# Performance work log

Measured on AMD Instinct MI355X. Metric: run time of the kernel, lower is better.

## Reference

```python
import jax, jax.numpy as jnp
import numpy as np

TOKEN_NUM = 81   # init default token_num
KNN_K = 2        # hardcoded in apply_clustering
LAYER_INDEX = 3


def setup_inputs() -> dict:
    key = jax.random.key(0)
    k1, k2, k3 = jax.random.split(key, 3)
    B, F, N, C = 8, 1024, 17, 512
    x = jax.random.normal(k1, (B, F, N, C), dtype=jnp.float32)
    # nn.Parameter init normal_(std=0.02)
    pos_embed_token = 0.02 * jax.random.normal(k2, (1, TOKEN_NUM, C), dtype=jnp.float32)
    # deterministic stand-in for torch.rand tie-breaker noise on density
    density_noise = jax.random.uniform(k3, (B, F), dtype=jnp.float32)
    return {"x": x, "pos_embed_token": pos_embed_token,
            "density_noise": density_noise, "current_layer": LAYER_INDEX}


def _dpc_knn_index(x_knn, density_noise, cluster_num, k):
    # x_knn: (B, F, C) pooled features; returns sorted cluster-center indices (B, cluster_num)
    B, F, C = x_knn.shape
    sq = jnp.sum(x_knn * x_knn, axis=-1)                       # (B, F)
    d2 = sq[:, :, None] + sq[:, None, :] - 2.0 * jnp.einsum('bic,bjc->bij', x_knn, x_knn)
    dist = jnp.sqrt(jnp.maximum(d2, 0.0)) / jnp.sqrt(jnp.asarray(C, x_knn.dtype))  # cdist / C**0.5
    # k smallest distances (self included, dist 0)
    neg_nearest, _ = jax.lax.top_k(-dist, k)                   # (B, F, k)
    dist_nearest = -neg_nearest
    density = jnp.exp(-jnp.mean(dist_nearest ** 2, axis=-1))   # (B, F)
    density = density + density_noise * 1e-6                   # tie-breaker
    # mask[b,i,j] = density[b,j] > density[b,i]
    mask = (density[:, None, :] > density[:, :, None]).astype(x_knn.dtype)
    dist_max = jnp.max(dist.reshape(B, -1), axis=-1)[:, None, None]
    min_dist = jnp.min(dist * mask + dist_max * (1.0 - mask), axis=-1)  # (B, F)
    score = min_dist * density
    _, index_down = jax.lax.top_k(score, cluster_num)          # (B, cluster_num)
    return jnp.sort(index_down, axis=-1)


def reference(x, pos_embed_token, density_noise, current_layer):
    # forward path only hits clustering when current_layer == layer_index
    if current_layer != LAYER_INDEX:
        return x
    B, F, N, C = x.shape
    # AdaptiveAvgPool1d(1) over joint axis after 'b f n c -> b (f c) n' == mean over n
    x_knn = jnp.mean(x, axis=2)                                # (B, F, C)
    index = _dpc_knn_index(x_knn, density_noise, TOKEN_NUM, KNN_K)
    index = jax.lax.stop_gradient(index)                       # clustering is under no_grad
    # gather selected frames: x[batch, index] -> (B, token_num, N, C)
    compressed = jnp.take_along_axis(x, index[:, :, None, None], axis=1)
    # '+ pos_embed_token' applied per (b n) f c  ==  broadcast over joints
    compressed = compressed + pos_embed_token[:, :, None, :]
    return compressed
```

## Files before the change

kernel.cpp:

```cpp
#include <hip/hip_runtime.h>
#include <math.h>
#include <float.h>

#define BB 8
#define FF 1024
#define NJ 17
#define CH 512
#define TOK 81
#define RCP_SQRT_C 0.04419417382415922f
#define LP 133

typedef short bf16x8 __attribute__((ext_vector_type(8)));
typedef float f32x16 __attribute__((ext_vector_type(16)));

static __device__ inline unsigned short f2bf(float f) {
    __bf16 h = (__bf16)f;
    return __builtin_bit_cast(unsigned short, h);
}
static __device__ inline float bf2f(unsigned short u) {
    return (float)__builtin_bit_cast(__bf16, u);
}


__global__ __launch_bounds__(256) void pool_kernel(const float* __restrict__ x,
                                                   uint4* __restrict__ fhi,
                                                   uint4* __restrict__ flo,
                                                   float* __restrict__ sq,
                                                   unsigned* __restrict__ ctrl) {
    const int t = threadIdx.x;
    if (blockIdx.x == 0 && t < 24) ctrl[t] = 0u;
    const int wid = t >> 6, lane = t & 63;
    const int row0 = blockIdx.x * 4;
    const int row = row0 + wid;
    const int b = row >> 10, f0 = row0 & 1023;
    const float* px = x + (size_t)row * NJ * CH + lane * 8;
    float a[8] = {};
    #pragma unroll
    for (int n = 0; n < NJ; ++n) {
        const float4 v0 = *(const float4*)(px + (size_t)n * CH);
        const float4 v1 = *(const float4*)(px + (size_t)n * CH + 4);
        a[0] += v0.x; a[1] += v0.y; a[2] += v0.z; a[3] += v0.w;
        a[4] += v1.x; a[5] += v1.y; a[6] += v1.z; a[7] += v1.w;
    }
    float ssq = 0.f;
    unsigned short hi[8], lo[8];
    #pragma unroll
    for (int j = 0; j < 8; ++j) {
        const float m = a[j] / 17.0f;
        ssq += m * m;
        hi[j] = f2bf(m);
        lo[j] = f2bf(m - bf2f(hi[j]));
    }
    #pragma unroll
    for (int off = 32; off > 0; off >>= 1) ssq += __shfl_down(ssq, off);
    if (lane == 0) sq[row] = ssq;

    uint4 uh, ul;
    uh.x = (unsigned)hi[0] | ((unsigned)hi[1] << 16);
    uh.y = (unsigned)hi[2] | ((unsigned)hi[3] << 16);
    uh.z = (unsigned)hi[4] | ((unsigned)hi[5] << 16);
    uh.w = (unsigned)hi[6] | ((unsigned)hi[7] << 16);
    ul.x = (unsigned)lo[0] | ((unsigned)lo[1] << 16);
    ul.y = (unsigned)lo[2] | ((unsigned)lo[3] << 16);
    ul.z = (unsigned)lo[4] | ((unsigned)lo[5] << 16);
    ul.w = (unsigned)lo[6] | ((unsigned)lo[7] << 16);
    __shared__ uint4 sh_hi[256], sh_lo[256];
    sh_hi[lane * 4 + wid] = uh;
    sh_lo[lane * 4 + wid] = ul;
    __syncthreads();
    const int k8 = t >> 2, fpr = t & 3;
    const int s = k8 >> 1, h = k8 & 1;
    const size_t o = (((size_t)b * 32 + s) * 2 + h) * 1024 + f0 + fpr;
    fhi[o] = sh_hi[t];
    flo[o] = sh_lo[t];
}

__global__ __launch_bounds__(256) void dist_kernel(const uint4* __restrict__ fhi,
                                                   const uint4* __restrict__ flo,
                                                   const float* __restrict__ sq,
                                                   float* __restrict__ dist) {
    const int b = blockIdx.x & 7;
    int tri = blockIdx.x >> 3, rt = 0;
    while (tri >= 8 - rt) { tri -= 8 - rt; ++rt; }
    const int ct = rt + tri;
    const bool diag = (rt == ct);
    const int tid = threadIdx.x;
    const int w = tid >> 6, lane = tid & 63;
    const int R = rt * 128 + (w & 1) * 64;
    const int C = ct * 128 + (w >> 1) * 64;
    const int h = lane >> 5, fr = lane & 31;

    size_t a0 = ((size_t)b * 64 + h) * 1024 + R + fr;
    size_t b0 = ((size_t)b * 64 + h) * 1024 + C + fr;

    f32x16 acc00, acc01, acc10, acc11;
    #pragma unroll
    for (int i = 0; i < 16; ++i) { acc00[i] = 0.f; acc01[i] = 0.f; acc10[i] = 0.f; acc11[i] = 0.f; }

    bf16x8 A0h = *(const bf16x8*)(fhi + a0), A1h = *(const bf16x8*)(fhi + a0 + 32);
    bf16x8 A0l = *(const bf16x8*)(flo + a0), A1l = *(const bf16x8*)(flo + a0 + 32);
    bf16x8 B0h = *(const bf16x8*)(fhi + b0), B1h = *(const bf16x8*)(fhi + b0 + 32);
    bf16x8 B0l = *(const bf16x8*)(flo + b0), B1l = *(const bf16x8*)(flo + b0 + 32);

    #pragma unroll 4
    for (int s = 0; s < 32; ++s) {
        const bf16x8 cA0h = A0h, cA1h = A1h, cA0l = A0l, cA1l = A1l;
        const bf16x8 cB0h = B0h, cB1h = B1h, cB0l = B0l, cB1l = B1l;
        if (s < 31) {
            a0 += 2048; b0 += 2048;
            A0h = *(const bf16x8*)(fhi + a0); A1h = *(const bf16x8*)(fhi + a0 + 32);
            A0l = *(const bf16x8*)(flo + a0); A1l = *(const bf16x8*)(flo + a0 + 32);
            B0h = *(const bf16x8*)(fhi + b0); B1h = *(const bf16x8*)(fhi + b0 + 32);
            B0l = *(const bf16x8*)(flo + b0); B1l = *(const bf16x8*)(flo + b0 + 32);
        }
        acc00 = __builtin_amdgcn_mfma_f32_32x32x16_bf16(cA0h, cB0h, acc00, 0, 0, 0);
        acc01 = __builtin_amdgcn_mfma_f32_32x32x16_bf16(cA0h, cB1h, acc01, 0, 0, 0);
        acc10 = __builtin_amdgcn_mfma_f32_32x32x16_bf16(cA1h, cB0h, acc10, 0, 0, 0);
        acc11 = __builtin_amdgcn_mfma_f32_32x32x16_bf16(cA1h, cB1h, acc11, 0, 0, 0);
        acc00 = __builtin_amdgcn_mfma_f32_32x32x16_bf16(cA0h, cB0l, acc00, 0, 0, 0);
        acc01 = __builtin_amdgcn_mfma_f32_32x32x16_bf16(cA0h, cB1l, acc01, 0, 0, 0);
        acc10 = __builtin_amdgcn_mfma_f32_32x32x16_bf16(cA1h, cB0l, acc10, 0, 0, 0);
        acc11 = __builtin_amdgcn_mfma_f32_32x32x16_bf16(cA1h, cB1l, acc11, 0, 0, 0);
        acc00 = __builtin_amdgcn_mfma_f32_32x32x16_bf16(cA0l, cB0h, acc00, 0, 0, 0);
        acc01 = __builtin_amdgcn_mfma_f32_32x32x16_bf16(cA0l, cB1h, acc01, 0, 0, 0);
        acc10 = __builtin_amdgcn_mfma_f32_32x32x16_bf16(cA1l, cB0h, acc10, 0, 0, 0);
        acc11 = __builtin_amdgcn_mfma_f32_32x32x16_bf16(cA1l, cB1h, acc11, 0, 0, 0);
    }

    __shared__ float lds[64 * LP];
    const int bF = b * FF;
    const int R0 = rt * 128, C0 = ct * 128;
    const float sqc0 = sq[bF + C + fr], sqc1 = sq[bF + C + fr + 32];
    const int lcb = (w >> 1) * 64 + fr;

    #pragma unroll
    for (int p = 0; p < 2; ++p) {
        if ((w & 1) == p) {
            #pragma unroll
            for (int reg = 0; reg < 16; ++reg) {
                const int rp = 4 * h + (reg & 3) + 8 * (reg >> 2);
                const float sqr0 = sq[bF + R + rp];
                const float sqr1 = sq[bF + R + rp + 32];
                lds[rp * LP + lcb] =
                    sqrtf(fmaxf(sqr0 + sqc0 - 2.0f * acc00[reg], 0.f)) * RCP_SQRT_C;
                lds[rp * LP + lcb + 32] =
                    sqrtf(fmaxf(sqr0 + sqc1 - 2.0f * acc01[reg], 0.f)) * RCP_SQRT_C;
                lds[(rp + 32) * LP + lcb] =
                    sqrtf(fmaxf(sqr1 + sqc0 - 2.0f * acc10[reg], 0.f)) * RCP_SQRT_C;
                lds[(rp + 32) * LP + lcb + 32] =
                    sqrtf(fmaxf(sqr1 + sqc1 - 2.0f * acc11[reg], 0.f)) * RCP_SQRT_C;
            }
        }
        __syncthreads();
        if (!diag) {
            for (int q = tid; q < 64 * 128; q += 256) {
                const int lr = q >> 7, c = q & 127;
                dist[((size_t)bF + R0 + p * 64 + lr) * FF + C0 + c] = lds[lr * LP + c];
            }
            for (int q = tid; q < 64 * 128; q += 256) {
                const int lr = q & 63, c = q >> 6;
                dist[((size_t)bF + C0 + c) * FF + R0 + p * 64 + lr] = lds[lr * LP + c];
            }
        } else if (p == 0) {
            for (int q = tid; q < 64 * 128; q += 256) {
                const int i = q >> 7, j = q & 127;
                const float v = (i == j) ? 0.f : (i < j ? lds[i * LP + j] : lds[j * LP + i]);
                dist[((size_t)bF + R0 + i) * FF + C0 + j] = v;
            }
            for (int q = tid; q < 64 * 64; q += 256) {
                const int i = 64 + (q >> 6), j = q & 63;
                dist[((size_t)bF + R0 + i) * FF + C0 + j] = lds[j * LP + i];
            }
        } else {
            for (int q = tid; q < 64 * 64; q += 256) {
                const int i = 64 + (q >> 6), j = 64 + (q & 63);
                const float v = (i == j) ? 0.f
                               : (i < j ? lds[(i - 64) * LP + j] : lds[(j - 64) * LP + i]);
                dist[((size_t)bF + R0 + i) * FF + C0 + j] = v;
            }
        }
        __syncthreads();
    }
}

__global__ __launch_bounds__(256) void stats_kernel(const float* __restrict__ dist,
                                                    const float* __restrict__ noise,
                                                    float* __restrict__ density,
                                                    unsigned* __restrict__ ctrl,
                                                    float* __restrict__ score,
                                                    int* __restrict__ selsort,
                                                    const float* __restrict__ x,
                                                    const float* __restrict__ pos,
                                                    float* __restrict__ out) {
    const int t = threadIdx.x, wid = t >> 6, lane = t & 63;
    const int g = blockIdx.x;
    const int b = g >> 5;
    unsigned* dmx = ctrl;
    unsigned* syncA = ctrl + 8;
    unsigned* syncD = ctrl + 9;
    unsigned* bcnt  = ctrl + 10;

    __shared__ float sdens[4][8];
    float wmax = -FLT_MAX;
    #pragma unroll
    for (int k = 0; k < 8; ++k) {
        const int r = g * 32 + wid * 8 + k;
        const int dcol = r & 1023;
        const float* dr = dist + (size_t)r * FF + lane * 4;
        float mn = FLT_MAX, mx = -FLT_MAX;
        #pragma unroll
        for (int j = 0; j < 4; ++j) {
            float4 d = *(const float4*)(dr + j * 256);
            mx = fmaxf(mx, fmaxf(fmaxf(d.x, d.y), fmaxf(d.z, d.w)));
            const int c0 = lane * 4 + j * 256;
            d.x = (c0 + 0 == dcol) ? FLT_MAX : d.x;
            d.y = (c0 + 1 == dcol) ? FLT_MAX : d.y;
            d.z = (c0 + 2 == dcol) ? FLT_MAX : d.z;
            d.w = (c0 + 3 == dcol) ? FLT_MAX : d.w;
            mn = fminf(mn, fminf(fminf(d.x, d.y), fminf(d.z, d.w)));
        }
        #pragma unroll
        for (int off = 32; off > 0; off >>= 1) {
            mn = fminf(mn, __shfl_down(mn, off));
            mx = fmaxf(mx, __shfl_down(mx, off));
        }
        if (lane == 0) {
            const float dv = expf(-0.5f * mn * mn) + noise[r] * 1e-6f;
            density[r] = dv;
            sdens[wid][k] = dv;
            wmax = fmaxf(wmax, mx);
        }
    }
    __shared__ float swm[4];
    if (lane == 0) swm[wid] = wmax;
    __syncthreads();
    if (t == 0) {
        atomicMax(&dmx[b], __float_as_uint(fmaxf(fmaxf(swm[0], swm[1]), fmaxf(swm[2], swm[3]))));
        __threadfence();
        atomicAdd(syncA, 1u);
        while (__hip_atomic_load(syncA, __ATOMIC_ACQUIRE, __HIP_MEMORY_SCOPE_AGENT) < 256u)
            __builtin_amdgcn_s_sleep(8);
    }
    __syncthreads();
    __threadfence();

    const float dmaxb = __uint_as_float(
        __hip_atomic_load(&dmx[b], __ATOMIC_RELAXED, __HIP_MEMORY_SCOPE_AGENT));
    float e[16];
    {
        const volatile float* db = density + (size_t)b * FF;
        #pragma unroll
        for (int j = 0; j < 16; ++j) e[j] = db[lane + j * 64];
    }
    #pragma unroll
    for (int k = 0; k < 8; ++k) {
        const int r = g * 32 + wid * 8 + k;
        const float dme = sdens[wid][k];
        const float* dr = dist + (size_t)r * FF;
        float mn = FLT_MAX;
        #pragma unroll
        for (int j = 0; j < 16; ++j) {
            const float d = dr[lane + j * 64];
            mn = fminf(mn, (e[j] > dme) ? d : FLT_MAX);
        }
        #pragma unroll
        for (int off = 32; off > 0; off >>= 1) mn = fminf(mn, __shfl_down(mn, off));
        if (lane == 0) score[r] = ((mn == FLT_MAX) ? dmaxb : mn) * dme;
    }
    __syncthreads();

    __shared__ int slast;
    if (t == 0) {
        __threadfence();
        slast = (atomicAdd(&bcnt[b], 1u) == 31u) ? 1 : 0;
    }
    __syncthreads();
    if (slast) {
        __threadfence();
        const volatile float* sb = score + (size_t)b * FF;
        unsigned v[4];
        #pragma unroll
        for (int j = 0; j < 4; ++j) v[j] = __float_as_uint(sb[t + 256 * j]);

        __shared__ unsigned hist[256];
        __shared__ unsigned wtot[4];
        __shared__ unsigned sh_byte, sh_kk;
        unsigned prefix = 0, kk = TOK;
        #pragma unroll
        for (int pass = 0; pass < 4; ++pass) {
            const int sh = 24 - 8 * pass;
            const unsigned pmask = (pass == 0) ? 0u : (0xFFFFFFFFu << (sh + 8));
            hist[t] = 0;
            __syncthreads();
            #pragma unroll
            for (int j = 0; j < 4; ++j)
                if ((v[j] & pmask) == prefix) atomicAdd(&hist[(v[j] >> sh) & 255], 1u);
            __syncthreads();
            const unsigned cnt = hist[t];
            unsigned s = cnt;
            #pragma unroll
            for (int off = 1; off < 64; off <<= 1) {
                const unsigned o = __shfl_down(s, off);
                if (lane + off < 64) s += o;
            }
            if (lane == 0) wtot[wid] = s;
            __syncthreads();
            unsigned hi2 = 0;
            for (int w2 = wid + 1; w2 < 4; ++w2) hi2 += wtot[w2];
            const unsigned S_incl = s + hi2;
            const unsigned S_excl = S_incl - cnt;
            if (S_excl < kk && kk <= S_incl) { sh_byte = (unsigned)t; sh_kk = kk - S_excl; }
            __syncthreads();
            prefix |= (sh_byte << sh);
            kk = sh_kk;
        }
        const unsigned T = prefix;

        __shared__ unsigned cgt[16], ceq[16];
        unsigned long long bgt[4], beq[4];
        #pragma unroll
        for (int j = 0; j < 4; ++j) {
            bgt[j] = __ballot(v[j] > T);
            beq[j] = __ballot(v[j] == T);
            if (lane == 0) {
                cgt[j * 4 + wid] = (unsigned)__popcll(bgt[j]);
                ceq[j * 4 + wid] = (unsigned)__popcll(beq[j]);
            }
        }
        __syncthreads();
        const unsigned long long below = (1ULL << lane) - 1ULL;
        #pragma unroll
        for (int j = 0; j < 4; ++j) {
            const bool gt = v[j] > T, eq = v[j] == T;
            if (!gt && !eq) continue;
            const int c = j * 4 + wid;
            unsigned bq_gt = 0, bq_eq = 0;
            for (int cc = 0; cc < c; ++cc) { bq_gt += cgt[cc]; bq_eq += ceq[cc]; }
            const unsigned wgt = (unsigned)__popcll(bgt[j] & below);
            const unsigned weq = (unsigned)__popcll(beq[j] & below);
            unsigned pos_;
            if (gt) {
                const unsigned eq_before = bq_eq + weq;
                pos_ = bq_gt + wgt + ((eq_before < kk) ? eq_before : kk);
            } else {
                const unsigned eord = bq_eq + weq;
                if (eord >= kk) continue;
                pos_ = bq_gt + wgt + eord;
            }
            selsort[b * TOK + pos_] = (int)(t + 256 * j);
        }
        __threadfence();
    }
    __syncthreads();
    if (t == 0) atomicAdd(syncD, 1u);

    if (t == 0) {
        while (__hip_atomic_load(syncD, __ATOMIC_ACQUIRE, __HIP_MEMORY_SCOPE_AGENT) < 256u)
            __builtin_amdgcn_s_sleep(8);
    }
    __syncthreads();
    __threadfence();

    __shared__ int ssel[BB * TOK];
    for (int q = t; q < BB * TOK; q += 256) ssel[q] = *((volatile const int*)selsort + q);
    __syncthreads();
    const size_t total = (size_t)BB * TOK * NJ * (CH / 4);
    for (size_t i = (size_t)g * 256 + t; i < total; i += 256 * 256) {
        const int c4 = (int)(i & (CH / 4 - 1));
        size_t r = i >> 7;
        const int n = (int)(r % NJ); r /= NJ;
        const int tok = (int)(r % TOK);
        const int bb = (int)(r / TOK);
        const int f = ssel[bb * TOK + tok];
        float4 v = *(const float4*)(x + (((size_t)(bb * FF + f)) * NJ + n) * CH + c4 * 4);
        const float4 p = *(const float4*)(pos + (size_t)tok * CH + c4 * 4);
        v.x += p.x; v.y += p.y; v.z += p.z; v.w += p.w;
        *(float4*)(out + i * 4) = v;
    }
}

extern "C" void kernel_launch(void* const* d_in, const int* in_sizes, int n_in,
                              void* d_out, int out_size, void* d_ws, size_t ws_size,
                              hipStream_t stream) {
    const float* x     = (const float*)d_in[0];
    const float* pos   = (const float*)d_in[1];
    const float* noise = (const float*)d_in[2];
    float* out = (float*)d_out;

    uint4* fhi    = (uint4*)d_ws;
    uint4* flo    = fhi + (size_t)BB * 32 * 2 * 1024;
    float* dist   = (float*)(flo + (size_t)BB * 32 * 2 * 1024);
    float* sq      = dist + (size_t)BB * FF * FF;
    float* density = sq + BB * FF;
    unsigned* ctrl = (unsigned*)(density + BB * FF);
    float* score   = (float*)(ctrl + 24);
    int*   selsort = (int*)(score + BB * FF);

    pool_kernel<<<(BB * FF) / 4, 256, 0, stream>>>(x, fhi, flo, sq, ctrl);
    dist_kernel<<<288, 256, 0, stream>>>(fhi, flo, sq, dist);
    stats_kernel<<<256, 256, 0, stream>>>(dist, noise, density, ctrl, score, selsort,
                                          x, pos, out);
}
```

Before: 563.6 us.

## Fuse nearest-neighbour min and global max into distance GEMM epilogue, split gather kernel

The distance kernel now computes each row's nearest non-self distance (via wave shuffles and atomicMin on float bits) and the per-batch maximum distance (atomicMax) directly from the MFMA accumulators. This removes the first pass over the full distance matrix and the grid-wide spin barrier from the stats kernel. The old persistent stats kernel is replaced by a per-row score kernel with a last-block top-k selection, followed by a separate fully parallel gather kernel that does not need a second grid barrier. The cost is many global atomics and an extra kernel launch.

```diff
diff --git a/kernel.cpp b/kernel.cpp
--- a/kernel.cpp
+++ b/kernel.cpp
@@ -20,17 +20,22 @@
 static __device__ inline float bf2f(unsigned short u) {
     return (float)__builtin_bit_cast(__bf16, u);
 }
+static __device__ __forceinline__ float densf(float rm, float nz) {
+    return expf(-0.5f * (rm * rm)) + nz * 1e-6f;
+}
 
 
 __global__ __launch_bounds__(256) void pool_kernel(const float* __restrict__ x,
                                                    uint4* __restrict__ fhi,
                                                    uint4* __restrict__ flo,
                                                    float* __restrict__ sq,
-                                                   unsigned* __restrict__ ctrl) {
+                                                   unsigned* __restrict__ ctrl,
+                                                   unsigned* __restrict__ rmin) {
     const int t = threadIdx.x;
-    if (blockIdx.x == 0 && t < 24) ctrl[t] = 0u;
+    const int row0 = blockIdx.x * 4;
+    if (t < 4) rmin[row0 + t] = 0x7F7FFFFFu;
+    if (blockIdx.x == 0 && t < 16) ctrl[t] = 0u;
     const int wid = t >> 6, lane = t & 63;
-    const int row0 = blockIdx.x * 4;
     const int row = row0 + wid;
     const int b = row >> 10, f0 = row0 & 1023;
     const float* px = x + (size_t)row * NJ * CH + lane * 8;
@@ -78,7 +83,9 @@
 __global__ __launch_bounds__(256) void dist_kernel(const uint4* __restrict__ fhi,
                                                    const uint4* __restrict__ flo,
                                                    const float* __restrict__ sq,
-                                                   float* __restrict__ dist) {
+                                                   float* __restrict__ dist,
+                                                   unsigned* __restrict__ ctrl,
+                                                   unsigned* __restrict__ rmin) {
     const int b = blockIdx.x & 7;
     int tri = blockIdx.x >> 3, rt = 0;
     while (tri >= 8 - rt) { tri -= 8 - rt; ++rt; }
@@ -127,10 +134,64 @@
         acc11 = __builtin_amdgcn_mfma_f32_32x32x16_bf16(cA1l, cB1h, acc11, 0, 0, 0);
     }
 
+    const int bF = b * FF;
+    const float sqc0 = sq[bF + C + fr], sqc1 = sq[bF + C + fr + 32];
+    #pragma unroll
+    for (int reg = 0; reg < 16; ++reg) {
+        const int rp = 4 * h + (reg & 3) + 8 * (reg >> 2);
+        const float sqr0 = sq[bF + R + rp];
+        const float sqr1 = sq[bF + R + rp + 32];
+        acc00[reg] = sqrtf(fmaxf(sqr0 + sqc0 - 2.0f * acc00[reg], 0.f)) * RCP_SQRT_C;
+        acc01[reg] = sqrtf(fmaxf(sqr0 + sqc1 - 2.0f * acc01[reg], 0.f)) * RCP_SQRT_C;
+        acc10[reg] = sqrtf(fmaxf(sqr1 + sqc0 - 2.0f * acc10[reg], 0.f)) * RCP_SQRT_C;
+        acc11[reg] = sqrtf(fmaxf(sqr1 + sqc1 - 2.0f * acc11[reg], 0.f)) * RCP_SQRT_C;
+    }
+
+    float mx = 0.f;
+    #pragma unroll
+    for (int reg = 0; reg < 16; ++reg) {
+        const int rp = 4 * h + (reg & 3) + 8 * (reg >> 2);
+        float w00 = acc00[reg], w01 = acc01[reg], w10 = acc10[reg], w11 = acc11[reg];
+        float x00 = w00, x01 = w01, x10 = w10, x11 = w11;
+        if (diag) {
+            if (C + fr == R + rp)           { w00 = FLT_MAX; x00 = 0.f; }
+            if (C + 32 + fr == R + rp)      { w01 = FLT_MAX; x01 = 0.f; }
+            if (C + fr == R + 32 + rp)      { w10 = FLT_MAX; x10 = 0.f; }
+            if (C + 32 + fr == R + 32 + rp) { w11 = FLT_MAX; x11 = 0.f; }
+        }
+        mx = fmaxf(mx, fmaxf(fmaxf(x00, x01), fmaxf(x10, x11)));
+        float r0 = fminf(w00, w01);
+        float r1 = fminf(w10, w11);
+        #pragma unroll
+        for (int off = 1; off < 32; off <<= 1) {
+            r0 = fminf(r0, __shfl_xor(r0, off));
+            r1 = fminf(r1, __shfl_xor(r1, off));
+        }
+        if (fr == 0) {
+            atomicMin(&rmin[bF + R + rp], __float_as_uint(r0));
+            atomicMin(&rmin[bF + R + 32 + rp], __float_as_uint(r1));
+        }
+    }
+    if (!diag) {
+        float c0 = FLT_MAX, c1 = FLT_MAX;
+        #pragma unroll
+        for (int reg = 0; reg < 16; ++reg) {
+            c0 = fminf(c0, fminf(acc00[reg], acc10[reg]));
+            c1 = fminf(c1, fminf(acc01[reg], acc11[reg]));
+        }
+        c0 = fminf(c0, __shfl_xor(c0, 32));
+        c1 = fminf(c1, __shfl_xor(c1, 32));
+        if (h == 0) {
+            atomicMin(&rmin[bF + C + fr], __float_as_uint(c0));
+            atomicMin(&rmin[bF + C + 32 + fr], __float_as_uint(c1));
+        }
+    }
+    #pragma unroll
+    for (int off = 1; off < 64; off <<= 1) mx = fmaxf(mx, __shfl_xor(mx, off));
+    if (lane == 0) atomicMax(&ctrl[b], __float_as_uint(mx));
+
     __shared__ float lds[64 * LP];
-    const int bF = b * FF;
     const int R0 = rt * 128, C0 = ct * 128;
-    const float sqc0 = sq[bF + C + fr], sqc1 = sq[bF + C + fr + 32];
     const int lcb = (w >> 1) * 64 + fr;
 
     #pragma unroll
@@ -139,16 +200,10 @@
             #pragma unroll
             for (int reg = 0; reg < 16; ++reg) {
                 const int rp = 4 * h + (reg & 3) + 8 * (reg >> 2);
-                const float sqr0 = sq[bF + R + rp];
-                const float sqr1 = sq[bF + R + rp + 32];
-                lds[rp * LP + lcb] =
-                    sqrtf(fmaxf(sqr0 + sqc0 - 2.0f * acc00[reg], 0.f)) * RCP_SQRT_C;
-                lds[rp * LP + lcb + 32] =
-                    sqrtf(fmaxf(sqr0 + sqc1 - 2.0f * acc01[reg], 0.f)) * RCP_SQRT_C;
-                lds[(rp + 32) * LP + lcb] =
-                    sqrtf(fmaxf(sqr1 + sqc0 - 2.0f * acc10[reg], 0.f)) * RCP_SQRT_C;
-                lds[(rp + 32) * LP + lcb + 32] =
-                    sqrtf(fmaxf(sqr1 + sqc1 - 2.0f * acc11[reg], 0.f)) * RCP_SQRT_C;
+                lds[rp * LP + lcb]            = acc00[reg];
+                lds[rp * LP + lcb + 32]       = acc01[reg];
+                lds[(rp + 32) * LP + lcb]     = acc10[reg];
+                lds[(rp + 32) * LP + lcb + 32] = acc11[reg];
             }
         }
         __syncthreads();
@@ -183,200 +238,174 @@
     }
 }
 
-__global__ __launch_bounds__(256) void stats_kernel(const float* __restrict__ dist,
-                                                    const float* __restrict__ noise,
-                                                    float* __restrict__ density,
-                                                    unsigned* __restrict__ ctrl,
-                                                    float* __restrict__ score,
-                                                    int* __restrict__ selsort,
-                                                    const float* __restrict__ x,
-                                                    const float* __restrict__ pos,
-                                                    float* __restrict__ out) {
+__global__ __launch_bounds__(256) void scoretop_kernel(const float* __restrict__ dist,
+                                                       const unsigned* __restrict__ rmin,
+                                                       const float* __restrict__ noise,
+                                                       unsigned* __restrict__ ctrl,
+                                                       float* __restrict__ score,
+                                                       int* __restrict__ selsort) {
     const int t = threadIdx.x, wid = t >> 6, lane = t & 63;
-    const int g = blockIdx.x;
-    const int b = g >> 5;
-    unsigned* dmx = ctrl;
-    unsigned* syncA = ctrl + 8;
-    unsigned* syncD = ctrl + 9;
-    unsigned* bcnt  = ctrl + 10;
-
-    __shared__ float sdens[4][8];
-    float wmax = -FLT_MAX;
-    #pragma unroll
-    for (int k = 0; k < 8; ++k) {
-        const int r = g * 32 + wid * 8 + k;
-        const int dcol = r & 1023;
-        const float* dr = dist + (size_t)r * FF + lane * 4;
-        float mn = FLT_MAX, mx = -FLT_MAX;
+    const int r = blockIdx.x * 4 + wid;
+    const int b = r >> 10, bF = b * FF;
+
+    float4 e0, e1, e2, e3;
+    #define MKE(EJ, J) { \
+        const uint4 rm = *(const uint4*)(rmin + bF + lane * 4 + (J) * 256); \
+        const float4 nz = *(const float4*)(noise + bF + lane * 4 + (J) * 256); \
+        EJ.x = densf(__uint_as_float(rm.x), nz.x); \
+        EJ.y = densf(__uint_as_float(rm.y), nz.y); \
+        EJ.z = densf(__uint_as_float(rm.z), nz.z); \
+        EJ.w = densf(__uint_as_float(rm.w), nz.w); }
+    MKE(e0, 0) MKE(e1, 1) MKE(e2, 2) MKE(e3, 3)
+    #undef MKE
+
+    const int dcol = r & 1023;
+    const int osel = ((dcol >> 8) << 2) | (dcol & 3);
+    const int olane = (dcol & 255) >> 2;
+    float own;
+    switch (osel) {
+        case 0:  own = e0.x; break; case 1:  own = e0.y; break;
+        case 2:  own = e0.z; break; case 3:  own = e0.w; break;
+        case 4:  own = e1.x; break; case 5:  own = e1.y; break;
+        case 6:  own = e1.z; break; case 7:  own = e1.w; break;
+        case 8:  own = e2.x; break; case 9:  own = e2.y; break;
+        case 10: own = e2.z; break; case 11: own = e2.w; break;
+        case 12: own = e3.x; break; case 13: own = e3.y; break;
+        case 14: own = e3.z; break; default: own = e3.w; break;
+    }
+    const float dme = __shfl(own, olane);
+
+    const float* dr = dist + (size_t)r * FF + lane * 4;
+    float mn = FLT_MAX;
+    {
+        const float4 d0 = *(const float4*)(dr);
+        const float4 d1 = *(const float4*)(dr + 256);
+        const float4 d2 = *(const float4*)(dr + 512);
+        const float4 d3 = *(const float4*)(dr + 768);
+        mn = fminf(mn, (e0.x > dme) ? d0.x : FLT_MAX);
+        mn = fminf(mn, (e0.y > dme) ? d0.y : FLT_MAX);
+        mn = fminf(mn, (e0.z > dme) ? d0.z : FLT_MAX);
+        mn = fminf(mn, (e0.w > dme) ? d0.w : FLT_MAX);
+        mn = fminf(mn, (e1.x > dme) ? d1.x : FLT_MAX);
+        mn = fminf(mn, (e1.y > dme) ? d1.y : FLT_MAX);
+        mn = fminf(mn, (e1.z > dme) ? d1.z : FLT_MAX);
+        mn = fminf(mn, (e1.w > dme) ? d1.w : FLT_MAX);
+        mn = fminf(mn, (e2.x > dme) ? d2.x : FLT_MAX);
+        mn = fminf(mn, (e2.y > dme) ? d2.y : FLT_MAX);
+        mn = fminf(mn, (e2.z > dme) ? d2.z : FLT_MAX);
+        mn = fminf(mn, (e2.w > dme) ? d2.w : FLT_MAX);
+        mn = fminf(mn, (e3.x > dme) ? d3.x : FLT_MAX);
+        mn = fminf(mn, (e3.y > dme) ? d3.y : FLT_MAX);
+        mn = fminf(mn, (e3.z > dme) ? d3.z : FLT_MAX);
+        mn = fminf(mn, (e3.w > dme) ? d3.w : FLT_MAX);
+    }
+    #pragma unroll
+    for (int off = 32; off > 0; off >>= 1) mn = fminf(mn, __shfl_down(mn, off));
+    if (lane == 0) {
+        const float dmaxb = __uint_as_float(ctrl[b]);
+        score[r] = ((mn == FLT_MAX) ? dmaxb : mn) * dme;
+        __threadfence();
+    }
+    __syncthreads();
+
+    __shared__ int slast;
+    unsigned* bcnt = ctrl + 8;
+    if (t == 0) slast = (atomicAdd(&bcnt[b], 1u) == 255u) ? 1 : 0;
+    __syncthreads();
+    if (!slast) return;
+    __threadfence();
+
+    const volatile float* sb = score + (size_t)b * FF;
+    unsigned v[4];
+    #pragma unroll
+    for (int j = 0; j < 4; ++j) v[j] = __float_as_uint(sb[t + 256 * j]);
+
+    __shared__ unsigned hist[256];
+    __shared__ unsigned wtot[4];
+    __shared__ unsigned sh_byte, sh_kk;
+    unsigned prefix = 0, kk = TOK;
+    #pragma unroll
+    for (int pass = 0; pass < 4; ++pass) {
+        const int sh = 24 - 8 * pass;
+        const unsigned pmask = (pass == 0) ? 0u : (0xFFFFFFFFu << (sh + 8));
+        hist[t] = 0;
+        __syncthreads();
         #pragma unroll
-        for (int j = 0; j < 4; ++j) {
-            float4 d = *(const float4*)(dr + j * 256);
-            mx = fmaxf(mx, fmaxf(fmaxf(d.x, d.y), fmaxf(d.z, d.w)));
-            const int c0 = lane * 4 + j * 256;
-            d.x = (c0 + 0 == dcol) ? FLT_MAX : d.x;
-            d.y = (c0 + 1 == dcol) ? FLT_MAX : d.y;
-            d.z = (c0 + 2 == dcol) ? FLT_MAX : d.z;
-            d.w = (c0 + 3 == dcol) ? FLT_MAX : d.w;
-            mn = fminf(mn, fminf(fminf(d.x, d.y), fminf(d.z, d.w)));
-        }
+        for (int j = 0; j < 4; ++j)
+            if ((v[j] & pmask) == prefix) atomicAdd(&hist[(v[j] >> sh) & 255], 1u);
+        __syncthreads();
+        const unsigned cnt = hist[t];
+        unsigned s = cnt;
         #pragma unroll
-        for (int off = 32; off > 0; off >>= 1) {
-            mn = fminf(mn, __shfl_down(mn, off));
-            mx = fmaxf(mx, __shfl_down(mx, off));
-        }
+        for (int off = 1; off < 64; off <<= 1) {
+            const unsigned o = __shfl_down(s, off);
+            if (lane + off < 64) s += o;
+        }
+        if (lane == 0) wtot[wid] = s;
+        __syncthreads();
+        unsigned hi2 = 0;
+        for (int w2 = wid + 1; w2 < 4; ++w2) hi2 += wtot[w2];
+        const unsigned S_incl = s + hi2;
+        const unsigned S_excl = S_incl - cnt;
+        if (S_excl < kk && kk <= S_incl) { sh_byte = (unsigned)t; sh_kk = kk - S_excl; }
+        __syncthreads();
+        prefix |= (sh_byte << sh);
+        kk = sh_kk;
+    }
+    const unsigned T = prefix;
+
+    __shared__ unsigned cgt[16], ceq[16];
+    unsigned long long bgt[4], beq[4];
+    #pragma unroll
+    for (int j = 0; j < 4; ++j) {
+        bgt[j] = __ballot(v[j] > T);
+        beq[j] = __ballot(v[j] == T);
         if (lane == 0) {
-            const float dv = expf(-0.5f * mn * mn) + noise[r] * 1e-6f;
-            density[r] = dv;
-            sdens[wid][k] = dv;
-            wmax = fmaxf(wmax, mx);
-        }
-    }
-    __shared__ float swm[4];
-    if (lane == 0) swm[wid] = wmax;
+            cgt[j * 4 + wid] = (unsigned)__popcll(bgt[j]);
+            ceq[j * 4 + wid] = (unsigned)__popcll(beq[j]);
+        }
+    }
     __syncthreads();
-    if (t == 0) {
-        atomicMax(&dmx[b], __float_as_uint(fmaxf(fmaxf(swm[0], swm[1]), fmaxf(swm[2], swm[3]))));
-        __threadfence();
-        atomicAdd(syncA, 1u);
-        while (__hip_atomic_load(syncA, __ATOMIC_ACQUIRE, __HIP_MEMORY_SCOPE_AGENT) < 256u)
-            __builtin_amdgcn_s_sleep(8);
-    }
-    __syncthreads();
-    __threadfence();
-
-    const float dmaxb = __uint_as_float(
-        __hip_atomic_load(&dmx[b], __ATOMIC_RELAXED, __HIP_MEMORY_SCOPE_AGENT));
-    float e[16];
-    {
-        const volatile float* db = density + (size_t)b * FF;
-        #pragma unroll
-        for (int j = 0; j < 16; ++j) e[j] = db[lane + j * 64];
-    }
-    #pragma unroll
-    for (int k = 0; k < 8; ++k) {
-        const int r = g * 32 + wid * 8 + k;
-        const float dme = sdens[wid][k];
-        const float* dr = dist + (size_t)r * FF;
-        float mn = FLT_MAX;
-        #pragma unroll
-        for (int j = 0; j < 16; ++j) {
-            const float d = dr[lane + j * 64];
-            mn = fminf(mn, (e[j] > dme) ? d : FLT_MAX);
-        }
-        #pragma unroll
-        for (int off = 32; off > 0; off >>= 1) mn = fminf(mn, __shfl_down(mn, off));
-        if (lane == 0) score[r] = ((mn == FLT_MAX) ? dmaxb : mn) * dme;
-    }
-    __syncthreads();
-
-    __shared__ int slast;
-    if (t == 0) {
-        __threadfence();
-        slast = (atomicAdd(&bcnt[b], 1u) == 31u) ? 1 : 0;
-    }
-    __syncthreads();
-    if (slast) {
-        __threadfence();
-        const volatile float* sb = score + (size_t)b * FF;
-        unsigned v[4];
-        #pragma unroll
-        for (int j = 0; j < 4; ++j) v[j] = __float_as_uint(sb[t + 256 * j]);
-
-        __shared__ unsigned hist[256];
-        __shared__ unsigned wtot[4];
-        __shared__ unsigned sh_byte, sh_kk;
-        unsigned prefix = 0, kk = TOK;
-        #pragma unroll
-        for (int pass = 0; pass < 4; ++pass) {
-            const int sh = 24 - 8 * pass;
-            const unsigned pmask = (pass == 0) ? 0u : (0xFFFFFFFFu << (sh + 8));
-            hist[t] = 0;
-            __syncthreads();
-            #pragma unroll
-            for (int j = 0; j < 4; ++j)
-                if ((v[j] & pmask) == prefix) atomicAdd(&hist[(v[j] >> sh) & 255], 1u);
-            __syncthreads();
-            const unsigned cnt = hist[t];
-            unsigned s = cnt;
-            #pragma unroll
-            for (int off = 1; off < 64; off <<= 1) {
-                const unsigned o = __shfl_down(s, off);
-                if (lane + off < 64) s += o;
-            }
-            if (lane == 0) wtot[wid] = s;
-            __syncthreads();
-            unsigned hi2 = 0;
-            for (int w2 = wid + 1; w2 < 4; ++w2) hi2 += wtot[w2];
-            const unsigned S_incl = s + hi2;
-            const unsigned S_excl = S_incl - cnt;
-            if (S_excl < kk && kk <= S_incl) { sh_byte = (unsigned)t; sh_kk = kk - S_excl; }
-            __syncthreads();
-            prefix |= (sh_byte << sh);
-            kk = sh_kk;
-        }
-        const unsigned T = prefix;
-
-        __shared__ unsigned cgt[16], ceq[16];
-        unsigned long long bgt[4], beq[4];
-        #pragma unroll
-        for (int j = 0; j < 4; ++j) {
-            bgt[j] = __ballot(v[j] > T);
-            beq[j] = __ballot(v[j] == T);
-            if (lane == 0) {
-                cgt[j * 4 + wid] = (unsigned)__popcll(bgt[j]);
-                ceq[j * 4 + wid] = (unsigned)__popcll(beq[j]);
-            }
-        }
-        __syncthreads();
-        const unsigned long long below = (1ULL << lane) - 1ULL;
-        #pragma unroll
-        for (int j = 0; j < 4; ++j) {
-            const bool gt = v[j] > T, eq = v[j] == T;
-            if (!gt && !eq) continue;
-            const int c = j * 4 + wid;
-            unsigned bq_gt = 0, bq_eq = 0;
-            for (int cc = 0; cc < c; ++cc) { bq_gt += cgt[cc]; bq_eq += ceq[cc]; }
-            const unsigned wgt = (unsigned)__popcll(bgt[j] & below);
-            const unsigned weq = (unsigned)__popcll(beq[j] & below);
-            unsigned pos_;
-            if (gt) {
-                const unsigned eq_before = bq_eq + weq;
-                pos_ = bq_gt + wgt + ((eq_before < kk) ? eq_before : kk);
-            } else {
-                const unsigned eord = bq_eq + weq;
-                if (eord >= kk) continue;
-                pos_ = bq_gt + wgt + eord;
-            }
-            selsort[b * TOK + pos_] = (int)(t + 256 * j);
-        }
-        __threadfence();
-    }
-    __syncthreads();
-    if (t == 0) atomicAdd(syncD, 1u);
-
-    if (t == 0) {
-        while (__hip_atomic_load(syncD, __ATOMIC_ACQUIRE, __HIP_MEMORY_SCOPE_AGENT) < 256u)
-            __builtin_amdgcn_s_sleep(8);
-    }
-    __syncthreads();
-    __threadfence();
-
-    __shared__ int ssel[BB * TOK];
-    for (int q = t; q < BB * TOK; q += 256) ssel[q] = *((volatile const int*)selsort + q);
-    __syncthreads();
+    const unsigned long long below = (1ULL << lane) - 1ULL;
+    #pragma unroll
+    for (int j = 0; j < 4; ++j) {
+        const bool gt = v[j] > T, eq = v[j] == T;
+        if (!gt && !eq) continue;
+        const int c = j * 4 + wid;
+        unsigned bq_gt = 0, bq_eq = 0;
+        for (int cc = 0; cc < c; ++cc) { bq_gt += cgt[cc]; bq_eq += ceq[cc]; }
+        const unsigned wgt = (unsigned)__popcll(bgt[j] & below);
+        const unsigned weq = (unsigned)__popcll(beq[j] & below);
+        unsigned pos_;
+        if (gt) {
+            const unsigned eq_before = bq_eq + weq;
+            pos_ = bq_gt + wgt + ((eq_before < kk) ? eq_before : kk);
+        } else {
+            const unsigned eord = bq_eq + weq;
+            if (eord >= kk) continue;
+            pos_ = bq_gt + wgt + eord;
+        }
+        selsort[b * TOK + pos_] = (int)(t + 256 * j);
+    }
+}
+
+__global__ __launch_bounds__(256) void gather_kernel(const float* __restrict__ x,
+                                                     const float* __restrict__ pos,
+                                                     const int* __restrict__ selsort,
+                                                     float* __restrict__ out) {
+    const size_t i = (size_t)blockIdx.x * 256 + threadIdx.x;
     const size_t total = (size_t)BB * TOK * NJ * (CH / 4);
-    for (size_t i = (size_t)g * 256 + t; i < total; i += 256 * 256) {
-        const int c4 = (int)(i & (CH / 4 - 1));
-        size_t r = i >> 7;
-        const int n = (int)(r % NJ); r /= NJ;
-        const int tok = (int)(r % TOK);
-        const int bb = (int)(r / TOK);
-        const int f = ssel[bb * TOK + tok];
-        float4 v = *(const float4*)(x + (((size_t)(bb * FF + f)) * NJ + n) * CH + c4 * 4);
-        const float4 p = *(const float4*)(pos + (size_t)tok * CH + c4 * 4);
-        v.x += p.x; v.y += p.y; v.z += p.z; v.w += p.w;
-        *(float4*)(out + i * 4) = v;
-    }
+    if (i >= total) return;
+    const int c4 = (int)(i & (CH / 4 - 1));
+    size_t r = i >> 7;
+    const int n = (int)(r % NJ); r /= NJ;
+    const int t = (int)(r % TOK);
+    const int b = (int)(r / TOK);
+    const int f = selsort[b * TOK + t];
+    float4 v = *(const float4*)(x + (((size_t)(b * FF + f)) * NJ + n) * CH + c4 * 4);
+    const float4 p = *(const float4*)(pos + (size_t)t * CH + c4 * 4);
+    v.x += p.x; v.y += p.y; v.z += p.z; v.w += p.w;
+    *(float4*)(out + i * 4) = v;
 }
 
 extern "C" void kernel_launch(void* const* d_in, const int* in_sizes, int n_in,
@@ -391,13 +420,14 @@
     uint4* flo    = fhi + (size_t)BB * 32 * 2 * 1024;
     float* dist   = (float*)(flo + (size_t)BB * 32 * 2 * 1024);
     float* sq      = dist + (size_t)BB * FF * FF;
-    float* density = sq + BB * FF;
-    unsigned* ctrl = (unsigned*)(density + BB * FF);
-    float* score   = (float*)(ctrl + 24);
+    unsigned* ctrl = (unsigned*)(sq + BB * FF);
+    unsigned* rmin = ctrl + 16;
+    float* score   = (float*)(rmin + BB * FF);
     int*   selsort = (int*)(score + BB * FF);
 
-    pool_kernel<<<(BB * FF) / 4, 256, 0, stream>>>(x, fhi, flo, sq, ctrl);
-    dist_kernel<<<288, 256, 0, stream>>>(fhi, flo, sq, dist);
-    stats_kernel<<<256, 256, 0, stream>>>(dist, noise, density, ctrl, score, selsort,
-                                          x, pos, out);
-}
+    pool_kernel<<<(BB * FF) / 4, 256, 0, stream>>>(x, fhi, flo, sq, ctrl, rmin);
+    dist_kernel<<<288, 256, 0, stream>>>(fhi, flo, sq, dist, ctrl, rmin);
+    scoretop_kernel<<<(BB * FF) / 4, 256, 0, stream>>>(dist, rmin, noise, ctrl, score, selsort);
+    const int gtot = (int)(((size_t)BB * TOK * NJ * (CH / 4) + 255) / 256);
+    gather_kernel<<<gtot, 256, 0, stream>>>(x, pos, selsort, out);
+}
```

New measurement: 707.6 us. +25.5%, slower.
